# Performance work log

Hardware: AMD Instinct MI355X
Metric: run time of the kernel (lower is better)

Reference implementation:

```python
import jax, jax.numpy as jnp
import numpy as np
from jax import lax

N, CI, CO, H, W = 2, 256, 256, 64, 64
K, G, DIL, PAD, STRIDE = 3, 8, 1, 1, 1
P = K * K
CG = CO // G  # group channels = 32


def setup_inputs() -> dict:
    key = jax.random.key(0)
    ks = jax.random.split(key, 24)
    r = lambda i, shape, s=1.0: jax.random.normal(ks[i], shape, jnp.float32) * s
    u = lambda i, shape: jax.random.uniform(ks[i], shape, jnp.float32, 0.5, 1.5)
    return dict(
        x=r(0, (N, CI, H, W)),
        conv1_w=r(1, (CO, CI), CI ** -0.5),
        bn1_g=u(2, (CO,)), bn1_b=r(3, (CO,), 0.1), bn1_m=r(4, (CO,), 0.1), bn1_v=u(5, (CO,)),
        inproj_w=r(6, (CO, CO), CO ** -0.5), inproj_b=r(7, (CO,), 0.02),
        dw_w=r(8, (CO, 1, K, K), 0.2), dw_b=r(9, (CO,), 0.02),
        ln_g=u(10, (CO,)), ln_b=r(11, (CO,), 0.02),
        off_w=r(12, (CO, G * P * 2), CO ** -0.5), off_b=jnp.zeros((G * P * 2,), jnp.float32),
        mask_w=r(13, (CO, G * P), CO ** -0.5), mask_b=jnp.zeros((G * P,), jnp.float32),
        outproj_w=r(14, (CO, CO), CO ** -0.5), outproj_b=r(15, (CO,), 0.02),
        bn2_g=u(16, (CO,)), bn2_b=r(17, (CO,), 0.1), bn2_m=r(18, (CO,), 0.1), bn2_v=u(19, (CO,)),
    )


def _bn(x, g, b, m, v, eps):
    # inference-mode BatchNorm2d on NCHW
    return (x - m[:, None, None]) * (g[:, None, None] * lax.rsqrt(v[:, None, None] + eps)) + b[:, None, None]


def _dcn_core(t, offset, mask):
    # t: (N,H,W,C) projected input; offset: (N,H,W,G*P*2); mask: (N,H,W,G,P) softmaxed
    xp = jnp.pad(t, ((0, 0), (PAD, PAD), (PAD, PAD), (0, 0)))
    H_, W_ = H + 2 * PAD, W + 2 * PAD
    # reference points (sample centers), normalized to padded size
    ry = ((DIL * (K - 1)) / 2 + 0.5 + STRIDE * jnp.arange(H, dtype=t.dtype)) / H_
    rx = ((DIL * (K - 1)) / 2 + 0.5 + STRIDE * jnp.arange(W, dtype=t.dtype)) / W_
    base = (DIL * (K - 1)) // 2
    gx = jnp.linspace(-base, -base + (K - 1) * DIL, K, dtype=t.dtype) / W_
    gy = jnp.linspace(-base, -base + (K - 1) * DIL, K, dtype=t.dtype) / H_
    gxx, gyy = jnp.meshgrid(gx, gy, indexing='ij')  # x varies along axis 0 (torch meshgrid order)
    grid = jnp.stack([gxx, gyy], -1).reshape(P, 2)  # (P,2)
    off = offset.reshape(N, H, W, G, P, 2) / jnp.array([W_, H_], t.dtype)
    loc_x = rx[None, None, :, None, None] + grid[:, 0][None, None, None, None] + off[..., 0]  # (N,H,W,G,P)
    loc_y = ry[None, :, None, None, None] + grid[:, 1][None, None, None, None] + off[..., 1]
    # grid_sample(align_corners=False): pixel = norm*size - 0.5
    px = jnp.transpose(loc_x * W_ - 0.5, (0, 3, 1, 2, 4)).reshape(N, G, H * W * P)
    py = jnp.transpose(loc_y * H_ - 0.5, (0, 3, 1, 2, 4)).reshape(N, G, H * W * P)
    # grouped channels-last image: (N,G,H_*W_,CG)
    xg = jnp.transpose(xp.reshape(N, H_, W_, G, CG), (0, 3, 1, 2, 4)).reshape(N, G, H_ * W_, CG)
    x0 = jnp.floor(px)
    y0 = jnp.floor(py)
    wx1 = px - x0
    wy1 = py - y0
    x0i = x0.astype(jnp.int32)
    y0i = y0.astype(jnp.int32)

    def corner(xi, yi, w):
        valid = (xi >= 0) & (xi <= W_ - 1) & (yi >= 0) & (yi <= H_ - 1)
        idx = jnp.clip(yi, 0, H_ - 1) * W_ + jnp.clip(xi, 0, W_ - 1)
        v = jnp.take_along_axis(xg, idx[..., None], axis=2)  # (N,G,M,CG)
        return v * jnp.where(valid, w, 0.0)[..., None]

    sampled = (corner(x0i, y0i, (1 - wx1) * (1 - wy1))
               + corner(x0i + 1, y0i, wx1 * (1 - wy1))
               + corner(x0i, y0i + 1, (1 - wx1) * wy1)
               + corner(x0i + 1, y0i + 1, wx1 * wy1))
    sampled = sampled.reshape(N, G, H * W, P, CG)
    mg = jnp.transpose(mask, (0, 3, 1, 2, 4)).reshape(N, G, H * W, P)
    out = jnp.einsum('nglpc,nglp->nglc', sampled, mg)
    return jnp.transpose(out, (0, 2, 1, 3)).reshape(N, H, W, G * CG)


def reference(x, conv1_w, bn1_g, bn1_b, bn1_m, bn1_v, inproj_w, inproj_b, dw_w, dw_b,
              ln_g, ln_b, off_w, off_b, mask_w, mask_b, outproj_w, outproj_b,
              bn2_g, bn2_b, bn2_m, bn2_v):
    # Conv(inc, ouc, k=1): 1x1 conv (no bias) + BN(eps=1e-3) + SiLU
    y = jnp.einsum('nchw,oc->nohw', x, conv1_w)
    y = jax.nn.silu(_bn(y, bn1_g, bn1_b, bn1_m, bn1_v, 1e-3))
    t = jnp.transpose(y, (0, 2, 3, 1))  # NHWC
    xproj = t @ inproj_w + inproj_b     # input_proj Linear
    # offset/mask branch: depthwise conv (k=3,s=1,p=1) -> LN over C -> GELU
    z = lax.conv_general_dilated(y, dw_w, (1, 1), ((PAD, PAD), (PAD, PAD)),
                                 feature_group_count=CO,
                                 dimension_numbers=('NCHW', 'OIHW', 'NCHW')) + dw_b[None, :, None, None]
    z = jnp.transpose(z, (0, 2, 3, 1))
    mu = jnp.mean(z, -1, keepdims=True)
    var = jnp.var(z, -1, keepdims=True)
    z = (z - mu) * lax.rsqrt(var + 1e-5) * ln_g + ln_b
    z = jax.nn.gelu(z, approximate=False)
    offset = z @ off_w + off_b  # (N,H,W,G*P*2)
    mask = jax.nn.softmax((z @ mask_w + mask_b).reshape(N, H, W, G, P), axis=-1)
    s = _dcn_core(xproj, offset, mask)
    s = s @ outproj_w + outproj_b  # output_proj Linear
    o = jnp.transpose(s, (0, 3, 1, 2))  # back to NCHW
    return jax.nn.silu(_bn(o, bn2_g, bn2_b, bn2_m, bn2_v, 1e-5))
```

## Files before the change

### kernel.cpp

```cpp
#include <hip/hip_runtime.h>
#include <hip/hip_fp16.h>
#include <math.h>

#define CC    256
#define HH    64
#define WW    64
#define HWSZ  4096
#define NPIX  8192
#define MT    16
#define TT    16
#define ASTR  264

typedef __attribute__((ext_vector_type(8))) _Float16 half8;
typedef __attribute__((ext_vector_type(4))) float f32x4;

__device__ __forceinline__ float silu_f(float x) { return x / (1.f + __expf(-x)); }

__device__ __forceinline__ short f2h(float f) {
    __half h = __float2half(f);
    return *reinterpret_cast<short*>(&h);
}
__device__ __forceinline__ unsigned h2u(float a, float b) {
    __half2 h = __floats2half2_rn(a, b);
    return *reinterpret_cast<unsigned*>(&h);
}
__device__ __forceinline__ __half2 u2h(unsigned v) { return *reinterpret_cast<__half2*>(&v); }
__device__ __forceinline__ unsigned h2raw(__half2 h) { return *reinterpret_cast<unsigned*>(&h); }
__device__ __forceinline__ float4 h2f4(uint2 u) {
    float2 a = __half22float2(u2h(u.x));
    float2 b = __half22float2(u2h(u.y));
    return make_float4(a.x, a.y, b.x, b.y);
}

__global__ void k_prep(const float* __restrict__ cw, const float* __restrict__ ipw,
                       const float* __restrict__ offw, const float* __restrict__ maskw,
                       const float* __restrict__ opw, const float* __restrict__ dww,
                       const float* __restrict__ offb, const float* __restrict__ maskb,
                       const float* __restrict__ g1, const float* __restrict__ b1,
                       const float* __restrict__ m1, const float* __restrict__ v1,
                       const float* __restrict__ g2, const float* __restrict__ b2,
                       const float* __restrict__ m2, const float* __restrict__ v2,
                       short* __restrict__ Wc1b, short* __restrict__ Wipb,
                       short* __restrict__ Whb, short* __restrict__ Wopb,
                       float* __restrict__ dwt,
                       float* __restrict__ bh, float* __restrict__ sc1, float* __restrict__ sh1,
                       float* __restrict__ sc2, float* __restrict__ sh2) {
    int o = blockIdx.x, c = threadIdx.x;
    Wc1b[o * CC + c] = f2h(cw[o * CC + c]);
    Wipb[o * CC + c] = f2h(ipw[c * CC + o]);
    float hv = 0.f;
    if (o < 144) hv = offw[c * 144 + o];
    else if (o < 216) hv = maskw[c * 72 + (o - 144)];
    Whb[o * CC + c] = f2h(hv);
    Wopb[o * CC + c] = f2h(opw[c * CC + o]);
    if (o < 9) dwt[o * CC + c] = dww[c * 9 + o];
    if (o == 0) {
        float bv = 0.f;
        if (c < 144) bv = offb[c];
        else if (c < 216) bv = maskb[c - 144];
        bh[c] = bv;
        float s1 = g1[c] * rsqrtf(v1[c] + 1e-3f);
        sc1[c] = s1; sh1[c] = b1[c] - m1[c] * s1;
        float s2 = g2[c] * rsqrtf(v2[c] + 1e-5f);
        sc2[c] = s2; sh2[c] = b2[c] - m2[c] * s2;
    }
}

__device__ __forceinline__ void gemm1(const short* As, const short* __restrict__ Wb,
                                      int lane, int n0, f32x4* acc) {
    const int m = lane & 15, q = lane >> 4;
#pragma unroll
    for (int kk = 0; kk < 8; ++kk) {
        int c0 = kk * 32 + q * 8;
        half8 a = *(const half8*)(As + m * ASTR + c0);
        half8 b = *(const half8*)(Wb + (size_t)(n0 + m) * CC + c0);
        *acc = __builtin_amdgcn_mfma_f32_16x16x32_f16(a, b, *acc, 0, 0, 0);
    }
}

__global__ __launch_bounds__(1024, 8) void k_conv_in(
        const float* __restrict__ x, const short* __restrict__ Wc1b,
        const short* __restrict__ Wipb, const float* __restrict__ sc1,
        const float* __restrict__ sh1, const float* __restrict__ ipb,
        short* __restrict__ ybf, short* __restrict__ xpb) {
    __shared__ __align__(16) short As[MT * ASTR];
    int tid = threadIdx.x, lane = tid & 63, wv = tid >> 6;
    int pix0 = blockIdx.x * MT;
    int n = pix0 >> 12, hw0 = pix0 & (HWSZ - 1);
    int n0 = wv * 16;
    const float* xn = x + (size_t)n * CC * HWSZ;
    {
        int c = tid >> 2, i4 = (tid & 3) * 4;
        float4 v = *(const float4*)(xn + (size_t)c * HWSZ + hw0 + i4);
        As[(i4 + 0) * ASTR + c] = f2h(v.x);
        As[(i4 + 1) * ASTR + c] = f2h(v.y);
        As[(i4 + 2) * ASTR + c] = f2h(v.z);
        As[(i4 + 3) * ASTR + c] = f2h(v.w);
    }
    __syncthreads();
    f32x4 acc = (f32x4){0.f, 0.f, 0.f, 0.f};
    gemm1(As, Wc1b, lane, n0, &acc);
    __syncthreads();
    int col = lane & 15, qr = (lane >> 4) * 4;
    int o = n0 + col;
    {
        float sc = sc1[o], sh = sh1[o];
#pragma unroll
        for (int r = 0; r < 4; ++r)
            As[(qr + r) * ASTR + o] = f2h(silu_f(acc[r] * sc + sh));
    }
    __syncthreads();
    *(uint2*)(ybf + (size_t)(pix0 + wv) * CC + lane * 4) =
        *(const uint2*)(As + wv * ASTR + lane * 4);
    acc = (f32x4){0.f, 0.f, 0.f, 0.f};
    gemm1(As, Wipb, lane, n0, &acc);
    __syncthreads();
    {
        float bo = ipb[o];
#pragma unroll
        for (int r = 0; r < 4; ++r)
            As[(qr + r) * ASTR + o] = f2h(acc[r] + bo);
    }
    __syncthreads();
    *(uint2*)(xpb + (size_t)(pix0 + wv) * CC + lane * 4) =
        *(const uint2*)(As + wv * ASTR + lane * 4);
}

__global__ __launch_bounds__(1024, 8) void k_tail(
        const short* __restrict__ ybf, const short* __restrict__ xpb,
        const float* __restrict__ dwt, const float* __restrict__ dwb,
        const float* __restrict__ lng, const float* __restrict__ lnb,
        const short* __restrict__ Whb, const float* __restrict__ bh,
        const short* __restrict__ Wopb, const float* __restrict__ opb,
        const float* __restrict__ sc2, const float* __restrict__ sh2,
        float* __restrict__ out) {
    __shared__ __align__(16) short As[TT * ASTR];
    __shared__ __align__(16) float buf[TT * 260];
    float* ml   = buf;
    float* loff = buf + 1536;
    float* xs   = buf;

    int tid = threadIdx.x, lane = tid & 63, wv = tid >> 6;
    int bid = blockIdx.x;
    int swz = ((bid & 7) << 6) | (bid >> 3);
    int pix0 = swz * TT;
    int n = pix0 >> 12, hw0 = pix0 & (HWSZ - 1);
    int h = hw0 >> 6, w0 = hw0 & 63;
    int c0 = lane * 4;
    int n0 = wv * 16;
    int col = lane & 15, qr = (lane >> 4) * 4;

    {
        float4 dwbv = *(const float4*)(dwb + c0);
        float4 lngv = *(const float4*)(lng + c0);
        float4 lnbv = *(const float4*)(lnb + c0);
        const short* yn = ybf + (size_t)n * HWSZ * CC;
        int pix = wv;
        int w = w0 + pix;
        float4 acc = dwbv;
        bool inter = (h > 0) && (h < HH - 1) && (w0 > 0) && (w0 < WW - TT);
        if (inter) {
#pragma unroll
            for (int ky = 0; ky < 3; ++ky) {
#pragma unroll
                for (int kx = 0; kx < 3; ++kx) {
                    int t = ky * 3 + kx;
                    float4 wt = *(const float4*)(dwt + t * CC + c0);
                    int idx = ((h + ky - 1) << 6) + (w + kx - 1);
                    float4 yv = h2f4(*(const uint2*)(yn + (size_t)idx * CC + c0));
                    acc.x += yv.x * wt.x;
                    acc.y += yv.y * wt.y;
                    acc.z += yv.z * wt.z;
                    acc.w += yv.w * wt.w;
                }
            }
        } else {
#pragma unroll
            for (int ky = 0; ky < 3; ++ky) {
                int yy = h + ky - 1;
                int yc = min(max(yy, 0), HH - 1);
                float vy = (yy == yc) ? 1.f : 0.f;
#pragma unroll
                for (int kx = 0; kx < 3; ++kx) {
                    int xx = w + kx - 1;
                    int xc = min(max(xx, 0), WW - 1);
                    float vm = vy * ((xx == xc) ? 1.f : 0.f);
                    int t = ky * 3 + kx;
                    float4 wt = *(const float4*)(dwt + t * CC + c0);
                    float4 yv = h2f4(*(const uint2*)(yn + (size_t)((yc << 6) + xc) * CC + c0));
                    acc.x += yv.x * wt.x * vm;
                    acc.y += yv.y * wt.y * vm;
                    acc.z += yv.z * wt.z * vm;
                    acc.w += yv.w * wt.w * vm;
                }
            }
        }
        float s1 = acc.x + acc.y + acc.z + acc.w;
        float s2 = acc.x * acc.x + acc.y * acc.y + acc.z * acc.z + acc.w * acc.w;
#pragma unroll
        for (int off = 32; off > 0; off >>= 1) {
            s1 += __shfl_xor(s1, off);
            s2 += __shfl_xor(s2, off);
        }
        float mu = s1 * (1.f / 256.f);
        float var = s2 * (1.f / 256.f) - mu * mu;
        float rs = rsqrtf(var + 1e-5f);
        float4 zv;
        zv.x = (acc.x - mu) * rs * lngv.x + lnbv.x;
        zv.y = (acc.y - mu) * rs * lngv.y + lnbv.y;
        zv.z = (acc.z - mu) * rs * lngv.z + lnbv.z;
        zv.w = (acc.w - mu) * rs * lngv.w + lnbv.w;
        zv.x = 0.5f * zv.x * (1.f + erff(zv.x * 0.70710678118654752f));
        zv.y = 0.5f * zv.y * (1.f + erff(zv.y * 0.70710678118654752f));
        zv.z = 0.5f * zv.z * (1.f + erff(zv.z * 0.70710678118654752f));
        zv.w = 0.5f * zv.w * (1.f + erff(zv.w * 0.70710678118654752f));
        *(uint2*)(As + pix * ASTR + c0) = make_uint2(h2u(zv.x, zv.y), h2u(zv.z, zv.w));
    }
    __syncthreads();

    {
        f32x4 acc = (f32x4){0.f, 0.f, 0.f, 0.f};
        gemm1(As, Whb, lane, n0, &acc);
        int o = n0 + col;
        float bo = bh[o];
#pragma unroll
        for (int r = 0; r < 4; ++r) {
            float v = acc[r] + bo;
            int pix = qr + r;
            if (o < 144) loff[pix * 144 + o] = v;
            else if (o < 216) {
                int mo = o - 144;
                int mg = (mo * 7282) >> 16;
                ml[pix * 96 + mg * 12 + (mo - mg * 9)] = v;
            }
        }
    }
    __syncthreads();

    {
        int g   = lane >> 3;
        int ci  = lane & 7;
        int cq  = ci & 3;
        int par = ci >> 2;
        int gc0 = g * 32 + cq * 8;
        int pix = wv;
        int w = w0 + pix;
        const float* row = ml + pix * 96 + g * 12;
        float4 r0 = *(const float4*)(row);
        float4 r1 = *(const float4*)(row + 4);
        float e0 = __expf(r0.x), e1 = __expf(r0.y), e2 = __expf(r0.z);
        float e3 = __expf(r0.w), e4 = __expf(r1.x), e5 = __expf(r1.y);
        float e6 = __expf(r1.z), e7 = __expf(r1.w), e8 = __expf(row[8]);
        float inv = 1.f / (e0 + e1 + e2 + e3 + e4 + e5 + e6 + e7 + e8);
        float m0 = (par ? e5 : e0) * inv;
        float m1 = (par ? e6 : e1) * inv;
        float m2 = (par ? e7 : e2) * inv;
        float m3 = (par ? e8 : e3) * inv;
        float m4 = e4 * inv;
        const float* lp = loff + pix * 144 + g * 18 + par * 10;
        const short* xpn = xpb + (size_t)n * HWSZ * CC;
        __half2 a0 = u2h(0u), a1 = u2h(0u), a2 = u2h(0u), a3 = u2h(0u);

        auto dotap = [&](float ox, float oy, int tx, int ty, float mval) {
            float px = (float)(w + tx) + ox;
            float py = (float)(h + ty) + oy;
            float fx = floorf(px), fy = floorf(py);
            float wx1 = px - fx, wy1 = py - fy;
            int x0 = (int)fx, y0 = (int)fy;
            int x1 = x0 + 1, y1 = y0 + 1;
            int xc0 = min(max(x0, 1), WW), xc1 = min(max(x1, 1), WW);
            int yc0 = min(max(y0, 1), HH), yc1 = min(max(y1, 1), HH);
            float vx0 = (x0 == xc0) ? 1.f : 0.f, vx1 = (x1 == xc1) ? 1.f : 0.f;
            float vy0 = (y0 == yc0) ? 1.f : 0.f, vy1 = (y1 == yc1) ? 1.f : 0.f;
            float w00 = (1.f - wx1) * (1.f - wy1) * mval * vx0 * vy0;
            float w10 = wx1 * (1.f - wy1) * mval * vx1 * vy0;
            float w01 = (1.f - wx1) * wy1 * mval * vx0 * vy1;
            float w11 = wx1 * wy1 * mval * vx1 * vy1;
            int i00 = (((yc0 - 1) << 6) + (xc0 - 1)) * CC + gc0;
            int i10 = (((yc0 - 1) << 6) + (xc1 - 1)) * CC + gc0;
            int i01 = (((yc1 - 1) << 6) + (xc0 - 1)) * CC + gc0;
            int i11 = (((yc1 - 1) << 6) + (xc1 - 1)) * CC + gc0;
            uint4 u00 = *(const uint4*)(xpn + i00);
            uint4 u10 = *(const uint4*)(xpn + i10);
            uint4 u01 = *(const uint4*)(xpn + i01);
            uint4 u11 = *(const uint4*)(xpn + i11);
            __half2 W00 = __float2half2_rn(w00);
            __half2 W10 = __float2half2_rn(w10);
            __half2 W01 = __float2half2_rn(w01);
            __half2 W11 = __float2half2_rn(w11);
            a0 = __hfma2(u2h(u00.x), W00, a0); a1 = __hfma2(u2h(u00.y), W00, a1);
            a2 = __hfma2(u2h(u00.z), W00, a2); a3 = __hfma2(u2h(u00.w), W00, a3);
            a0 = __hfma2(u2h(u10.x), W10, a0); a1 = __hfma2(u2h(u10.y), W10, a1);
            a2 = __hfma2(u2h(u10.z), W10, a2); a3 = __hfma2(u2h(u10.w), W10, a3);
            a0 = __hfma2(u2h(u01.x), W01, a0); a1 = __hfma2(u2h(u01.y), W01, a1);
            a2 = __hfma2(u2h(u01.z), W01, a2); a3 = __hfma2(u2h(u01.w), W01, a3);
            a0 = __hfma2(u2h(u11.x), W11, a0); a1 = __hfma2(u2h(u11.y), W11, a1);
            a2 = __hfma2(u2h(u11.z), W11, a2); a3 = __hfma2(u2h(u11.w), W11, a3);
        };

        {
            float2 of;
            of = *(const float2*)(lp + 0);
            dotap(of.x, of.y, par ? 1 : 0, par ? 2 : 0, m0);
            of = *(const float2*)(lp + 2);
            dotap(of.x, of.y, par ? 2 : 0, par ? 0 : 1, m1);
            of = *(const float2*)(lp + 4);
            dotap(of.x, of.y, par ? 2 : 0, par ? 1 : 2, m2);
            of = *(const float2*)(lp + 6);
            dotap(of.x, of.y, par ? 2 : 1, par ? 2 : 0, m3);
            if (!par) {
                of = *(const float2*)(lp + 8);
                dotap(of.x, of.y, 1, 1, m4);
            }
        }
        a0 = __hadd2(a0, u2h((unsigned)__shfl_xor((int)h2raw(a0), 4)));
        a1 = __hadd2(a1, u2h((unsigned)__shfl_xor((int)h2raw(a1), 4)));
        a2 = __hadd2(a2, u2h((unsigned)__shfl_xor((int)h2raw(a2), 4)));
        a3 = __hadd2(a3, u2h((unsigned)__shfl_xor((int)h2raw(a3), 4)));
        if (!par)
            *(uint4*)(As + pix * ASTR + gc0) =
                make_uint4(h2raw(a0), h2raw(a1), h2raw(a2), h2raw(a3));
    }
    __syncthreads();

    {
        f32x4 acc = (f32x4){0.f, 0.f, 0.f, 0.f};
        gemm1(As, Wopb, lane, n0, &acc);
        int o = n0 + col;
        float bo = opb[o], sc = sc2[o], sh = sh2[o];
#pragma unroll
        for (int r = 0; r < 4; ++r)
            xs[(qr + r) * 260 + o] = silu_f((acc[r] + bo) * sc + sh);
    }
    __syncthreads();

    {
        int i4 = (tid & 3) * 4;
        int o = tid >> 2;
        float* on = out + (size_t)n * CC * HWSZ + hw0 + i4;
        float4 ov;
        ov.x = xs[(i4 + 0) * 260 + o];
        ov.y = xs[(i4 + 1) * 260 + o];
        ov.z = xs[(i4 + 2) * 260 + o];
        ov.w = xs[(i4 + 3) * 260 + o];
        *(float4*)(on + (size_t)o * HWSZ) = ov;
    }
}

extern "C" void kernel_launch(void* const* d_in, const int* in_sizes, int n_in,
                              void* d_out, int out_size, void* d_ws, size_t ws_size,
                              hipStream_t stream) {
    const float* x        = (const float*)d_in[0];
    const float* conv1_w  = (const float*)d_in[1];
    const float* bn1_g    = (const float*)d_in[2];
    const float* bn1_b    = (const float*)d_in[3];
    const float* bn1_m    = (const float*)d_in[4];
    const float* bn1_v    = (const float*)d_in[5];
    const float* inproj_w = (const float*)d_in[6];
    const float* inproj_b = (const float*)d_in[7];
    const float* dw_w     = (const float*)d_in[8];
    const float* dw_b     = (const float*)d_in[9];
    const float* ln_g     = (const float*)d_in[10];
    const float* ln_b     = (const float*)d_in[11];
    const float* off_w    = (const float*)d_in[12];
    const float* off_b    = (const float*)d_in[13];
    const float* mask_w   = (const float*)d_in[14];
    const float* mask_b   = (const float*)d_in[15];
    const float* outproj_w = (const float*)d_in[16];
    const float* outproj_b = (const float*)d_in[17];
    const float* bn2_g    = (const float*)d_in[18];
    const float* bn2_b    = (const float*)d_in[19];
    const float* bn2_m    = (const float*)d_in[20];
    const float* bn2_v    = (const float*)d_in[21];
    float* out = (float*)d_out;

    short* Wc1b = (short*)d_ws;
    short* Wipb = Wc1b + 65536;
    short* Whb  = Wipb + 65536;
    short* Wopb = Whb + 65536;
    float* fp   = (float*)(Wopb + 65536);
    float* dwt  = fp;
    float* bh   = dwt + 9 * CC;
    float* sc1  = bh + 256;
    float* sh1  = sc1 + 256;
    float* sc2  = sh1 + 256;
    float* sh2  = sc2 + 256;
    short* ybf  = (short*)(sh2 + 256);
    short* xpb  = ybf + (size_t)NPIX * CC;

    k_prep<<<dim3(CC), dim3(CC), 0, stream>>>(conv1_w, inproj_w, off_w, mask_w, outproj_w, dw_w,
                                              off_b, mask_b, bn1_g, bn1_b, bn1_m, bn1_v,
                                              bn2_g, bn2_b, bn2_m, bn2_v,
                                              Wc1b, Wipb, Whb, Wopb, dwt, bh, sc1, sh1, sc2, sh2);
    k_conv_in<<<dim3(NPIX / MT), dim3(1024), 0, stream>>>(x, Wc1b, Wipb, sc1, sh1, inproj_b, ybf, xpb);
    k_tail<<<dim3(NPIX / TT), dim3(1024), 0, stream>>>(ybf, xpb, dwt, dw_b, ln_g, ln_b,
                                                       Whb, bh, Wopb, outproj_b, sc2, sh2, out);
}
```

Measured before the change: 158.1 us.

## Tile weight prep via LDS transpose, double conv_in pixel tile, batch tap gathers

The weight prep kernel now transposes the weight matrices through shared-memory tiles using 53 blocks, and converts conv1 with vector stores, replacing 256 blocks that did strided reads. The input conv kernel handles 32 pixels per block, so each weight fragment it loads feeds two MFMAs, and it writes results straight to global memory instead of staging them through LDS, which removes some barriers. The deformable sampling loop now computes indices for two taps and issues all eight gathers before the FMAs, to get more memory-level parallelism. The direct global stores from conv_in are less coalesced, since they are per-column short writes.

```diff
diff --git a/kernel.cpp b/kernel.cpp
--- a/kernel.cpp
+++ b/kernel.cpp
@@ -7,7 +7,7 @@
 #define WW    64
 #define HWSZ  4096
 #define NPIX  8192
-#define MT    16
+#define MT    32
 #define TT    16
 #define ASTR  264
 
@@ -32,29 +32,58 @@
     return make_float4(a.x, a.y, b.x, b.y);
 }
 
-__global__ void k_prep(const float* __restrict__ cw, const float* __restrict__ ipw,
-                       const float* __restrict__ offw, const float* __restrict__ maskw,
-                       const float* __restrict__ opw, const float* __restrict__ dww,
-                       const float* __restrict__ offb, const float* __restrict__ maskb,
-                       const float* __restrict__ g1, const float* __restrict__ b1,
-                       const float* __restrict__ m1, const float* __restrict__ v1,
-                       const float* __restrict__ g2, const float* __restrict__ b2,
-                       const float* __restrict__ m2, const float* __restrict__ v2,
-                       short* __restrict__ Wc1b, short* __restrict__ Wipb,
-                       short* __restrict__ Whb, short* __restrict__ Wopb,
-                       float* __restrict__ dwt,
-                       float* __restrict__ bh, float* __restrict__ sc1, float* __restrict__ sh1,
-                       float* __restrict__ sc2, float* __restrict__ sh2) {
-    int o = blockIdx.x, c = threadIdx.x;
-    Wc1b[o * CC + c] = f2h(cw[o * CC + c]);
-    Wipb[o * CC + c] = f2h(ipw[c * CC + o]);
-    float hv = 0.f;
-    if (o < 144) hv = offw[c * 144 + o];
-    else if (o < 216) hv = maskw[c * 72 + (o - 144)];
-    Whb[o * CC + c] = f2h(hv);
-    Wopb[o * CC + c] = f2h(opw[c * CC + o]);
-    if (o < 9) dwt[o * CC + c] = dww[c * 9 + o];
-    if (o == 0) {
+__global__ __launch_bounds__(256) void k_prep(
+        const float* __restrict__ cw, const float* __restrict__ ipw,
+        const float* __restrict__ offw, const float* __restrict__ maskw,
+        const float* __restrict__ opw, const float* __restrict__ dww,
+        const float* __restrict__ offb, const float* __restrict__ maskb,
+        const float* __restrict__ g1, const float* __restrict__ b1,
+        const float* __restrict__ m1, const float* __restrict__ v1,
+        const float* __restrict__ g2, const float* __restrict__ b2,
+        const float* __restrict__ m2, const float* __restrict__ v2,
+        short* __restrict__ Wc1b, short* __restrict__ Wipb,
+        short* __restrict__ Whb, short* __restrict__ Wopb,
+        float* __restrict__ dwt,
+        float* __restrict__ bh, float* __restrict__ sc1, float* __restrict__ sh1,
+        float* __restrict__ sc2, float* __restrict__ sh2) {
+    __shared__ float tile[64 * 65];
+    int t = threadIdx.x, bt = blockIdx.x;
+    int ct = t & 63, rb = t >> 6;
+    if (bt < 48) {
+        int m = bt >> 4;
+        int sub = bt & 15;
+        int oT = (sub & 3) * 64, cT = (sub >> 2) * 64;
+        const float* src = (m == 0) ? ipw : opw;
+#pragma unroll
+        for (int i = 0; i < 16; ++i) {
+            int r = rb * 16 + i;
+            int c = cT + r, o = oT + ct;
+            float v;
+            if (m < 2) v = src[c * CC + o];
+            else v = (o < 144) ? offw[c * 144 + o]
+                   : (o < 216) ? maskw[c * 72 + (o - 144)] : 0.f;
+            tile[r * 65 + ct] = v;
+        }
+        __syncthreads();
+        short* dst = (m == 0) ? Wipb : (m == 1) ? Wopb : Whb;
+#pragma unroll
+        for (int i = 0; i < 16; ++i) {
+            int r = rb * 16 + i;
+            dst[(size_t)(oT + r) * CC + cT + ct] = f2h(tile[ct * 65 + r]);
+        }
+    } else if (bt < 52) {
+        int base = (bt - 48) * 16384;
+#pragma unroll
+        for (int i = 0; i < 16; ++i) {
+            int idx = base + i * 1024 + t * 4;
+            float4 v = *(const float4*)(cw + idx);
+            *(uint2*)(Wc1b + idx) = make_uint2(h2u(v.x, v.y), h2u(v.z, v.w));
+        }
+    } else {
+        int c = t;
+#pragma unroll
+        for (int j = 0; j < 9; ++j)
+            dwt[j * CC + c] = dww[c * 9 + j];
         float bv = 0.f;
         if (c < 144) bv = offb[c];
         else if (c < 216) bv = maskb[c - 144];
@@ -89,41 +118,49 @@
     int n = pix0 >> 12, hw0 = pix0 & (HWSZ - 1);
     int n0 = wv * 16;
     const float* xn = x + (size_t)n * CC * HWSZ;
-    {
-        int c = tid >> 2, i4 = (tid & 3) * 4;
-        float4 v = *(const float4*)(xn + (size_t)c * HWSZ + hw0 + i4);
-        As[(i4 + 0) * ASTR + c] = f2h(v.x);
-        As[(i4 + 1) * ASTR + c] = f2h(v.y);
-        As[(i4 + 2) * ASTR + c] = f2h(v.z);
-        As[(i4 + 3) * ASTR + c] = f2h(v.w);
-    }
-    __syncthreads();
-    f32x4 acc = (f32x4){0.f, 0.f, 0.f, 0.f};
-    gemm1(As, Wc1b, lane, n0, &acc);
+#pragma unroll
+    for (int rep = 0; rep < 2; ++rep) {
+        int f = tid + rep * 1024;
+        int c = f >> 3, i8 = (f & 7) * 4;
+        float4 v = *(const float4*)(xn + (size_t)c * HWSZ + hw0 + i8);
+        As[(i8 + 0) * ASTR + c] = f2h(v.x);
+        As[(i8 + 1) * ASTR + c] = f2h(v.y);
+        As[(i8 + 2) * ASTR + c] = f2h(v.z);
+        As[(i8 + 3) * ASTR + c] = f2h(v.w);
+    }
+    __syncthreads();
+    f32x4 acc0 = (f32x4){0.f, 0.f, 0.f, 0.f};
+    f32x4 acc1 = (f32x4){0.f, 0.f, 0.f, 0.f};
+    gemm1(As, Wc1b, lane, n0, &acc0);
+    gemm1(As + 16 * ASTR, Wc1b, lane, n0, &acc1);
     __syncthreads();
     int col = lane & 15, qr = (lane >> 4) * 4;
     int o = n0 + col;
     {
         float sc = sc1[o], sh = sh1[o];
 #pragma unroll
-        for (int r = 0; r < 4; ++r)
-            As[(qr + r) * ASTR + o] = f2h(silu_f(acc[r] * sc + sh));
-    }
-    __syncthreads();
-    *(uint2*)(ybf + (size_t)(pix0 + wv) * CC + lane * 4) =
-        *(const uint2*)(As + wv * ASTR + lane * 4);
-    acc = (f32x4){0.f, 0.f, 0.f, 0.f};
-    gemm1(As, Wipb, lane, n0, &acc);
-    __syncthreads();
+        for (int r = 0; r < 4; ++r) {
+            short v0 = f2h(silu_f(acc0[r] * sc + sh));
+            As[(qr + r) * ASTR + o] = v0;
+            ybf[(size_t)(pix0 + qr + r) * CC + o] = v0;
+            short v1 = f2h(silu_f(acc1[r] * sc + sh));
+            As[(16 + qr + r) * ASTR + o] = v1;
+            ybf[(size_t)(pix0 + 16 + qr + r) * CC + o] = v1;
+        }
+    }
+    __syncthreads();
+    acc0 = (f32x4){0.f, 0.f, 0.f, 0.f};
+    acc1 = (f32x4){0.f, 0.f, 0.f, 0.f};
+    gemm1(As, Wipb, lane, n0, &acc0);
+    gemm1(As + 16 * ASTR, Wipb, lane, n0, &acc1);
     {
         float bo = ipb[o];
 #pragma unroll
-        for (int r = 0; r < 4; ++r)
-            As[(qr + r) * ASTR + o] = f2h(acc[r] + bo);
-    }
-    __syncthreads();
-    *(uint2*)(xpb + (size_t)(pix0 + wv) * CC + lane * 4) =
-        *(const uint2*)(As + wv * ASTR + lane * 4);
+        for (int r = 0; r < 4; ++r) {
+            xpb[(size_t)(pix0 + qr + r) * CC + o] = f2h(acc0[r] + bo);
+            xpb[(size_t)(pix0 + 16 + qr + r) * CC + o] = f2h(acc1[r] + bo);
+        }
+    }
 }
 
 __global__ __launch_bounds__(1024, 8) void k_tail(
@@ -261,7 +298,9 @@
         const short* xpn = xpb + (size_t)n * HWSZ * CC;
         __half2 a0 = u2h(0u), a1 = u2h(0u), a2 = u2h(0u), a3 = u2h(0u);
 
-        auto dotap = [&](float ox, float oy, int tx, int ty, float mval) {
+        auto tapw = [&](float ox, float oy, int tx, int ty, float mval,
+                        int& i00, int& i10, int& i01, int& i11,
+                        float& w00, float& w10, float& w01, float& w11) {
             float px = (float)(w + tx) + ox;
             float py = (float)(h + ty) + oy;
             float fx = floorf(px), fy = floorf(py);
@@ -272,46 +311,65 @@
             int yc0 = min(max(y0, 1), HH), yc1 = min(max(y1, 1), HH);
             float vx0 = (x0 == xc0) ? 1.f : 0.f, vx1 = (x1 == xc1) ? 1.f : 0.f;
             float vy0 = (y0 == yc0) ? 1.f : 0.f, vy1 = (y1 == yc1) ? 1.f : 0.f;
-            float w00 = (1.f - wx1) * (1.f - wy1) * mval * vx0 * vy0;
-            float w10 = wx1 * (1.f - wy1) * mval * vx1 * vy0;
-            float w01 = (1.f - wx1) * wy1 * mval * vx0 * vy1;
-            float w11 = wx1 * wy1 * mval * vx1 * vy1;
-            int i00 = (((yc0 - 1) << 6) + (xc0 - 1)) * CC + gc0;
-            int i10 = (((yc0 - 1) << 6) + (xc1 - 1)) * CC + gc0;
-            int i01 = (((yc1 - 1) << 6) + (xc0 - 1)) * CC + gc0;
-            int i11 = (((yc1 - 1) << 6) + (xc1 - 1)) * CC + gc0;
-            uint4 u00 = *(const uint4*)(xpn + i00);
-            uint4 u10 = *(const uint4*)(xpn + i10);
-            uint4 u01 = *(const uint4*)(xpn + i01);
-            uint4 u11 = *(const uint4*)(xpn + i11);
-            __half2 W00 = __float2half2_rn(w00);
-            __half2 W10 = __float2half2_rn(w10);
-            __half2 W01 = __float2half2_rn(w01);
-            __half2 W11 = __float2half2_rn(w11);
-            a0 = __hfma2(u2h(u00.x), W00, a0); a1 = __hfma2(u2h(u00.y), W00, a1);
-            a2 = __hfma2(u2h(u00.z), W00, a2); a3 = __hfma2(u2h(u00.w), W00, a3);
-            a0 = __hfma2(u2h(u10.x), W10, a0); a1 = __hfma2(u2h(u10.y), W10, a1);
-            a2 = __hfma2(u2h(u10.z), W10, a2); a3 = __hfma2(u2h(u10.w), W10, a3);
-            a0 = __hfma2(u2h(u01.x), W01, a0); a1 = __hfma2(u2h(u01.y), W01, a1);
-            a2 = __hfma2(u2h(u01.z), W01, a2); a3 = __hfma2(u2h(u01.w), W01, a3);
-            a0 = __hfma2(u2h(u11.x), W11, a0); a1 = __hfma2(u2h(u11.y), W11, a1);
-            a2 = __hfma2(u2h(u11.z), W11, a2); a3 = __hfma2(u2h(u11.w), W11, a3);
+            w00 = (1.f - wx1) * (1.f - wy1) * mval * vx0 * vy0;
+            w10 = wx1 * (1.f - wy1) * mval * vx1 * vy0;
+            w01 = (1.f - wx1) * wy1 * mval * vx0 * vy1;
+            w11 = wx1 * wy1 * mval * vx1 * vy1;
+            i00 = (((yc0 - 1) << 6) + (xc0 - 1)) * CC + gc0;
+            i10 = (((yc0 - 1) << 6) + (xc1 - 1)) * CC + gc0;
+            i01 = (((yc1 - 1) << 6) + (xc0 - 1)) * CC + gc0;
+            i11 = (((yc1 - 1) << 6) + (xc1 - 1)) * CC + gc0;
         };
-
+        auto fma4 = [&](uint4 u, float wgt) {
+            __half2 W = __float2half2_rn(wgt);
+            a0 = __hfma2(u2h(u.x), W, a0);
+            a1 = __hfma2(u2h(u.y), W, a1);
+            a2 = __hfma2(u2h(u.z), W, a2);
+            a3 = __hfma2(u2h(u.w), W, a3);
+        };
+
+        int A00, A10, A01, A11, B00, B10, B01, B11;
+        float Wa0, Wa1, Wa2, Wa3, Wb0, Wb1, Wb2, Wb3;
+        float2 ofa = *(const float2*)(lp + 0);
+        float2 ofb = *(const float2*)(lp + 2);
+        tapw(ofa.x, ofa.y, par ? 1 : 0, par ? 2 : 0, m0, A00, A10, A01, A11, Wa0, Wa1, Wa2, Wa3);
+        tapw(ofb.x, ofb.y, par ? 2 : 0, par ? 0 : 1, m1, B00, B10, B01, B11, Wb0, Wb1, Wb2, Wb3);
         {
-            float2 of;
-            of = *(const float2*)(lp + 0);
-            dotap(of.x, of.y, par ? 1 : 0, par ? 2 : 0, m0);
-            of = *(const float2*)(lp + 2);
-            dotap(of.x, of.y, par ? 2 : 0, par ? 0 : 1, m1);
-            of = *(const float2*)(lp + 4);
-            dotap(of.x, of.y, par ? 2 : 0, par ? 1 : 2, m2);
-            of = *(const float2*)(lp + 6);
-            dotap(of.x, of.y, par ? 2 : 1, par ? 2 : 0, m3);
-            if (!par) {
-                of = *(const float2*)(lp + 8);
-                dotap(of.x, of.y, 1, 1, m4);
-            }
+            uint4 uA0 = *(const uint4*)(xpn + A00);
+            uint4 uA1 = *(const uint4*)(xpn + A10);
+            uint4 uA2 = *(const uint4*)(xpn + A01);
+            uint4 uA3 = *(const uint4*)(xpn + A11);
+            uint4 uB0 = *(const uint4*)(xpn + B00);
+            uint4 uB1 = *(const uint4*)(xpn + B10);
+            uint4 uB2 = *(const uint4*)(xpn + B01);
+            uint4 uB3 = *(const uint4*)(xpn + B11);
+            fma4(uA0, Wa0); fma4(uA1, Wa1); fma4(uA2, Wa2); fma4(uA3, Wa3);
+            fma4(uB0, Wb0); fma4(uB1, Wb1); fma4(uB2, Wb2); fma4(uB3, Wb3);
+        }
+        ofa = *(const float2*)(lp + 4);
+        ofb = *(const float2*)(lp + 6);
+        tapw(ofa.x, ofa.y, par ? 2 : 0, par ? 1 : 2, m2, A00, A10, A01, A11, Wa0, Wa1, Wa2, Wa3);
+        tapw(ofb.x, ofb.y, par ? 2 : 1, par ? 2 : 0, m3, B00, B10, B01, B11, Wb0, Wb1, Wb2, Wb3);
+        {
+            uint4 uA0 = *(const uint4*)(xpn + A00);
+            uint4 uA1 = *(const uint4*)(xpn + A10);
+            uint4 uA2 = *(const uint4*)(xpn + A01);
+            uint4 uA3 = *(const uint4*)(xpn + A11);
+            uint4 uB0 = *(const uint4*)(xpn + B00);
+            uint4 uB1 = *(const uint4*)(xpn + B10);
+            uint4 uB2 = *(const uint4*)(xpn + B01);
+            uint4 uB3 = *(const uint4*)(xpn + B11);
+            fma4(uA0, Wa0); fma4(uA1, Wa1); fma4(uA2, Wa2); fma4(uA3, Wa3);
+            fma4(uB0, Wb0); fma4(uB1, Wb1); fma4(uB2, Wb2); fma4(uB3, Wb3);
+        }
+        if (!par) {
+            ofa = *(const float2*)(lp + 8);
+            tapw(ofa.x, ofa.y, 1, 1, m4, A00, A10, A01, A11, Wa0, Wa1, Wa2, Wa3);
+            uint4 uA0 = *(const uint4*)(xpn + A00);
+            uint4 uA1 = *(const uint4*)(xpn + A10);
+            uint4 uA2 = *(const uint4*)(xpn + A01);
+            uint4 uA3 = *(const uint4*)(xpn + A11);
+            fma4(uA0, Wa0); fma4(uA1, Wa1); fma4(uA2, Wa2); fma4(uA3, Wa3);
         }
         a0 = __hadd2(a0, u2h((unsigned)__shfl_xor((int)h2raw(a0), 4)));
         a1 = __hadd2(a1, u2h((unsigned)__shfl_xor((int)h2raw(a1), 4)));
@@ -388,10 +446,10 @@
     short* ybf  = (short*)(sh2 + 256);
     short* xpb  = ybf + (size_t)NPIX * CC;
 
-    k_prep<<<dim3(CC), dim3(CC), 0, stream>>>(conv1_w, inproj_w, off_w, mask_w, outproj_w, dw_w,
-                                              off_b, mask_b, bn1_g, bn1_b, bn1_m, bn1_v,
-                                              bn2_g, bn2_b, bn2_m, bn2_v,
-                                              Wc1b, Wipb, Whb, Wopb, dwt, bh, sc1, sh1, sc2, sh2);
+    k_prep<<<dim3(53), dim3(256), 0, stream>>>(conv1_w, inproj_w, off_w, mask_w, outproj_w, dw_w,
+                                               off_b, mask_b, bn1_g, bn1_b, bn1_m, bn1_v,
+                                               bn2_g, bn2_b, bn2_m, bn2_v,
+                                               Wc1b, Wipb, Whb, Wopb, dwt, bh, sc1, sh1, sc2, sh2);
     k_conv_in<<<dim3(NPIX / MT), dim3(1024), 0, stream>>>(x, Wc1b, Wipb, sc1, sh1, inproj_b, ybf, xpb);
     k_tail<<<dim3(NPIX / TT), dim3(1024), 0, stream>>>(ybf, xpb, dwt, dw_b, ln_g, ln_b,
                                                        Whb, bh, Wopb, outproj_b, sc2, sh2, out);
```

Result: faster. 153.0 us (-3.2%).
